# Kernel tuning notes

Hardware: AMD Instinct MI355X
Metric: run time of the kernel (lower is better)

## Reference

```python
import jax, jax.numpy as jnp
import numpy as np

HC = 4
C = 256
TMAX = 20
RMS_EPS = 1e-6
PRE_EPS = 0.0
SINKHORN_EPS = 1e-6
POST_MULT = 2.0


def setup_inputs() -> dict:
    key = jax.random.key(0)
    k1, k2, k3 = jax.random.split(key, 3)
    B, S = 8, 4096
    m = HC * HC + 2 * HC
    x = jax.random.normal(k1, (B, S, HC, C), dtype=jnp.float32)
    phi = jax.random.normal(k2, (HC * C, m), dtype=jnp.float32) * 0.02
    b = jnp.zeros((m,), dtype=jnp.float32)
    W = jax.random.normal(k3, (C, C), dtype=jnp.float32) * (1.0 / np.sqrt(C))
    return {
        "x": x, "phi": phi, "b": b,
        "alpha_pre": jnp.float32(1.0), "alpha_post": jnp.float32(1.0), "alpha_res": jnp.float32(1.0),
        "W": W,
    }


def _mhc_coeffs(x, phi, b, alpha_pre, alpha_post, alpha_res):
    # x: [..., HC, C] -> flatten streams, project, RMS-normalize logits.
    lead = x.shape[:-2]
    v = x.reshape(lead + (HC * C,))
    logits = jnp.einsum('...k,km->...m', v, phi)            # [..., m]
    rms = jnp.sqrt(jnp.mean(logits * logits, axis=-1, keepdims=True) + RMS_EPS)
    y = logits / rms + b                                     # [..., m]
    pre = y[..., :HC]
    post = y[..., HC:2 * HC]
    res = y[..., 2 * HC:].reshape(lead + (HC, HC))
    h_pre = jax.nn.sigmoid(alpha_pre * pre) + PRE_EPS        # [..., HC]
    h_post = POST_MULT * jax.nn.sigmoid(alpha_post * post)   # [..., HC]
    # Sinkhorn-Knopp: make exp(alpha_res * res) approximately doubly stochastic.
    P = jnp.exp(alpha_res * res)                             # [..., HC, HC]

    def step(P, _):
        P = P / (jnp.sum(P, axis=-1, keepdims=True) + SINKHORN_EPS)  # row norm
        P = P / (jnp.sum(P, axis=-2, keepdims=True) + SINKHORN_EPS)  # col norm
        return P, None

    P, _ = jax.lax.scan(step, P, None, length=TMAX)
    return h_pre, h_post, P


def reference(x, phi, b, alpha_pre, alpha_post, alpha_res, W):
    h_pre, h_post, h_res = _mhc_coeffs(x, phi, b, alpha_pre, alpha_post, alpha_res)
    # Pre-aggregate streams: x_in = sum_i h_pre[i] * x[i]
    x_in = jnp.einsum('...i,...ic->...c', h_pre, x)          # [..., C]
    # Wrapped layer: nn.Linear(C, C, bias=False) -> x_in @ W.T
    f_out = x_in @ W.T                                       # [..., C]
    # Post + residual: x_out[o] = sum_i h_res[o,i]*x[i] + h_post[o]*f_out
    x_out = jnp.einsum('...oi,...ic->...oc', h_res, x) + h_post[..., :, None] * f_out[..., None, :]
    return x_out
```

## Files before the change

kernel.cpp:

```cpp
#include <hip/hip_runtime.h>

typedef __attribute__((ext_vector_type(4))) float floatx4;
typedef __attribute__((ext_vector_type(8))) short short8;

__device__ __forceinline__ unsigned short f2bf(float f) {
    union { float f; unsigned int i; } v; v.f = f;
    unsigned int x = v.i;
    unsigned int r = (x + 0x7FFFu + ((x >> 16) & 1u)) >> 16;
    return (unsigned short)r;
}
__device__ __forceinline__ float bf2f(unsigned short u) {
    union { unsigned int i; float f; } v; v.i = ((unsigned int)u) << 16;
    return v.f;
}

__global__ void mhc_prep(const float* __restrict__ phi, const float* __restrict__ W,
                         unsigned short* __restrict__ phiF, unsigned short* __restrict__ WF) {
    int e = blockIdx.x * 256 + threadIdx.x;
    if (e < 32768) {
        int j = e & 7, lane = (e >> 3) & 63, nt = (e >> 9) & 1, ks = e >> 10;
        int n = nt * 16 + (lane & 15);
        int k = ks * 32 + ((lane >> 4) & 3) * 8 + j;
        float v = (n < 24) ? phi[k * 24 + n] : 0.0f;
        phiF[e] = f2bf(v);
    } else {
        int e2 = e - 32768;
        int j = e2 & 7, lane = (e2 >> 3) & 63, ks = (e2 >> 9) & 7, nt = e2 >> 12;
        int n = nt * 16 + (lane & 15);
        int k = ks * 32 + ((lane >> 4) & 3) * 8 + j;
        WF[e2] = f2bf(W[n * 256 + k]);
    }
}

#define XS_STRIDE 1032
#define XIN_STRIDE 264
#define CO_STRIDE 28

__global__ __launch_bounds__(256) void mhc_main(
    const float* __restrict__ x, const float* __restrict__ bias,
    const float* __restrict__ s_ap, const float* __restrict__ s_apo,
    const float* __restrict__ s_ar,
    const unsigned short* __restrict__ phiF, const unsigned short* __restrict__ WF,
    float* __restrict__ out)
{
    __shared__ unsigned short xs[16 * XS_STRIDE];
    __shared__ unsigned short xin[16 * XIN_STRIDE];
    __shared__ float lg[16 * CO_STRIDE];
    __shared__ float coef[16 * CO_STRIDE];

    const int t = threadIdx.x;
    const int lane = t & 63;
    const int w = t >> 6;
    const int quad = lane >> 4;
    const int col = lane & 15;
    const long base = (long)blockIdx.x * (16 * 1024);

    {
        const float4* xg = (const float4*)(x + base);
        #pragma unroll
        for (int ii = 0; ii < 16; ++ii) {
            int lin = ii * 256 + t;
            float4 v = xg[lin];
            int tok = lin >> 8;
            int k = (lin & 255) * 4;
            uint2 pk;
            pk.x = (unsigned int)f2bf(v.x) | ((unsigned int)f2bf(v.y) << 16);
            pk.y = (unsigned int)f2bf(v.z) | ((unsigned int)f2bf(v.w) << 16);
            *reinterpret_cast<uint2*>(&xs[tok * XS_STRIDE + k]) = pk;
        }
    }
    __syncthreads();

    if (w < 2) {
        floatx4 acc = {0.0f, 0.0f, 0.0f, 0.0f};
        for (int ks = 0; ks < 32; ++ks) {
            short8 a = *reinterpret_cast<const short8*>(&xs[col * XS_STRIDE + ks * 32 + quad * 8]);
            short8 b = *reinterpret_cast<const short8*>(&phiF[(ks * 2 + w) * 512 + lane * 8]);
            acc = __builtin_amdgcn_mfma_f32_16x16x32_bf16(a, b, acc, 0, 0, 0);
        }
        int n = w * 16 + col;
        if (n < 24) {
            #pragma unroll
            for (int r = 0; r < 4; ++r)
                lg[(quad * 4 + r) * CO_STRIDE + n] = acc[r];
        }
    }
    __syncthreads();

    {
        int g = t >> 4, p = t & 15;
        float a = lg[g * CO_STRIDE + p];
        float b2 = (p < 8) ? lg[g * CO_STRIDE + 16 + p] : 0.0f;
        float s = a * a + b2 * b2;
        s += __shfl_xor(s, 1); s += __shfl_xor(s, 2);
        s += __shfl_xor(s, 4); s += __shfl_xor(s, 8);
        float rinv = 1.0f / sqrtf(s * (1.0f / 24.0f) + 1e-6f);
        float yP = lg[g * CO_STRIDE + 8 + p] * rinv + bias[8 + p];
        float P = expf(s_ar[0] * yP);
        for (int it = 0; it < 20; ++it) {
            float r = P + __shfl_xor(P, 1); r += __shfl_xor(r, 2);
            P *= __builtin_amdgcn_rcpf(r + 1e-6f);
            float c = P + __shfl_xor(P, 4); c += __shfl_xor(c, 8);
            P *= __builtin_amdgcn_rcpf(c + 1e-6f);
        }
        coef[g * CO_STRIDE + 8 + p] = P;
        if (p < 8) {
            float yh = a * rinv + bias[p];
            float h = (p < 4) ? 1.0f / (1.0f + expf(-s_ap[0] * yh))
                              : 2.0f / (1.0f + expf(-s_apo[0] * yh));
            coef[g * CO_STRIDE + p] = h;
        }
    }
    __syncthreads();

    {
        int c = t;
        #pragma unroll 4
        for (int tok = 0; tok < 16; ++tok) {
            float4 h4 = *reinterpret_cast<const float4*>(&coef[tok * CO_STRIDE]);
            const unsigned short* xr = &xs[tok * XS_STRIDE + c];
            float s = h4.x * bf2f(xr[0]) + h4.y * bf2f(xr[256])
                    + h4.z * bf2f(xr[512]) + h4.w * bf2f(xr[768]);
            xin[tok * XIN_STRIDE + c] = f2bf(s);
        }
    }
    __syncthreads();

    short8 afr[8];
    #pragma unroll
    for (int ks = 0; ks < 8; ++ks)
        afr[ks] = *reinterpret_cast<const short8*>(&xin[col * XIN_STRIDE + ks * 32 + quad * 8]);
    floatx4 accs[4];
    #pragma unroll
    for (int nt = 0; nt < 4; ++nt) {
        floatx4 acc = {0.0f, 0.0f, 0.0f, 0.0f};
        int ntile = w * 4 + nt;
        #pragma unroll
        for (int ks = 0; ks < 8; ++ks) {
            short8 b = *reinterpret_cast<const short8*>(&WF[(ntile * 8 + ks) * 512 + lane * 8]);
            acc = __builtin_amdgcn_mfma_f32_16x16x32_bf16(afr[ks], b, acc, 0, 0, 0);
        }
        accs[nt] = acc;
    }

    #pragma unroll
    for (int r = 0; r < 4; ++r) {
        int tok = quad * 4 + r;
        const float* cb = &coef[tok * CO_STRIDE];
        float4 hpo = *reinterpret_cast<const float4*>(cb + 4);
        float4 P0  = *reinterpret_cast<const float4*>(cb + 8);
        float4 P1  = *reinterpret_cast<const float4*>(cb + 12);
        float4 P2  = *reinterpret_cast<const float4*>(cb + 16);
        float4 P3  = *reinterpret_cast<const float4*>(cb + 20);
        long ob = base + (long)tok * 1024;
        #pragma unroll
        for (int nt = 0; nt < 4; ++nt) {
            int c = (w * 4 + nt) * 16 + col;
            float f = accs[nt][r];
            const unsigned short* xr = &xs[tok * XS_STRIDE + c];
            float x0 = bf2f(xr[0]),   x1 = bf2f(xr[256]);
            float x2 = bf2f(xr[512]), x3 = bf2f(xr[768]);
            out[ob + c]       = P0.x * x0 + P0.y * x1 + P0.z * x2 + P0.w * x3 + hpo.x * f;
            out[ob + 256 + c] = P1.x * x0 + P1.y * x1 + P1.z * x2 + P1.w * x3 + hpo.y * f;
            out[ob + 512 + c] = P2.x * x0 + P2.y * x1 + P2.z * x2 + P2.w * x3 + hpo.z * f;
            out[ob + 768 + c] = P3.x * x0 + P3.y * x1 + P3.z * x2 + P3.w * x3 + hpo.w * f;
        }
    }
}

extern "C" void kernel_launch(void* const* d_in, const int* in_sizes, int n_in,
                              void* d_out, int out_size, void* d_ws, size_t ws_size,
                              hipStream_t stream) {
    const float* x    = (const float*)d_in[0];
    const float* phi  = (const float*)d_in[1];
    const float* bias = (const float*)d_in[2];
    const float* ap   = (const float*)d_in[3];
    const float* apo  = (const float*)d_in[4];
    const float* ar   = (const float*)d_in[5];
    const float* W    = (const float*)d_in[6];
    float* out = (float*)d_out;

    unsigned short* phiF = (unsigned short*)d_ws;
    unsigned short* WF   = (unsigned short*)d_ws + 32768;

    mhc_prep<<<384, 256, 0, stream>>>(phi, W, phiF, WF);
    mhc_main<<<2048, 256, 0, stream>>>(x, bias, ap, apo, ar, phiF, WF, out);
}
```

Before: 262.9 us.

## Keep x in fp32 registers, split logits GEMM across warps, vectorize output stores

Each warp now loads four tokens of x into fp32 registers and reuses them for both pre-aggregation and the residual mix. This removes the bf16 LDS round trip and improves accuracy. The logits GEMM is split over all four warps along K, with partial sums added afterwards. Sinkhorn now runs on 4 lanes per token, each holding one row in registers, so row sums need no shuffles. The GEMM output is staged through LDS that aliases the x buffer, so the epilogue can write contiguous float4 nontemporal stores. The cost is more register pressure (launch_bounds 256,3) and extra barriers.

```diff
diff --git a/kernel.cpp b/kernel.cpp
--- a/kernel.cpp
+++ b/kernel.cpp
@@ -1,17 +1,22 @@
 #include <hip/hip_runtime.h>
+#include <hip/hip_bf16.h>
 
 typedef __attribute__((ext_vector_type(4))) float floatx4;
 typedef __attribute__((ext_vector_type(8))) short short8;
 
 __device__ __forceinline__ unsigned short f2bf(float f) {
     union { float f; unsigned int i; } v; v.f = f;
-    unsigned int x = v.i;
-    unsigned int r = (x + 0x7FFFu + ((x >> 16) & 1u)) >> 16;
+    unsigned int r = (v.i + 0x7FFFu + ((v.i >> 16) & 1u)) >> 16;
     return (unsigned short)r;
 }
-__device__ __forceinline__ float bf2f(unsigned short u) {
-    union { unsigned int i; float f; } v; v.i = ((unsigned int)u) << 16;
-    return v.f;
+
+__device__ __forceinline__ uint2 pack_bf16x4(float4 v) {
+    __hip_bfloat162 lo = __float22bfloat162_rn(make_float2(v.x, v.y));
+    __hip_bfloat162 hi = __float22bfloat162_rn(make_float2(v.z, v.w));
+    uint2 r;
+    __builtin_memcpy(&r.x, &lo, 4);
+    __builtin_memcpy(&r.y, &hi, 4);
+    return r;
 }
 
 __global__ void mhc_prep(const float* __restrict__ phi, const float* __restrict__ W,
@@ -21,8 +26,7 @@
         int j = e & 7, lane = (e >> 3) & 63, nt = (e >> 9) & 1, ks = e >> 10;
         int n = nt * 16 + (lane & 15);
         int k = ks * 32 + ((lane >> 4) & 3) * 8 + j;
-        float v = (n < 24) ? phi[k * 24 + n] : 0.0f;
-        phiF[e] = f2bf(v);
+        phiF[e] = f2bf((n < 24) ? phi[k * 24 + n] : 0.0f);
     } else {
         int e2 = e - 32768;
         int j = e2 & 7, lane = (e2 >> 3) & 63, ks = (e2 >> 9) & 7, nt = e2 >> 12;
@@ -34,137 +38,180 @@
 
 #define XS_STRIDE 1032
 #define XIN_STRIDE 264
-#define CO_STRIDE 28
-
-__global__ __launch_bounds__(256) void mhc_main(
+#define FO_STRIDE 260
+#define CO_STRIDE 24
+
+__global__ __launch_bounds__(256, 3) void mhc_main(
     const float* __restrict__ x, const float* __restrict__ bias,
     const float* __restrict__ s_ap, const float* __restrict__ s_apo,
     const float* __restrict__ s_ar,
     const unsigned short* __restrict__ phiF, const unsigned short* __restrict__ WF,
     float* __restrict__ out)
 {
-    __shared__ unsigned short xs[16 * XS_STRIDE];
-    __shared__ unsigned short xin[16 * XIN_STRIDE];
-    __shared__ float lg[16 * CO_STRIDE];
-    __shared__ float coef[16 * CO_STRIDE];
+    __shared__ __align__(16) unsigned char smem[16 * XS_STRIDE * 2];
+    __shared__ __align__(16) float lgp[2][16 * CO_STRIDE];
+    __shared__ __align__(16) float lgy[16 * CO_STRIDE];
+    __shared__ __align__(16) float coef[16 * CO_STRIDE];
+
+    unsigned short* xs  = (unsigned short*)smem;
+    unsigned short* xin = (unsigned short*)smem;
+    float*          fo  = (float*)(smem + 16 * XIN_STRIDE * 2);
 
     const int t = threadIdx.x;
     const int lane = t & 63;
     const int w = t >> 6;
     const int quad = lane >> 4;
     const int col = lane & 15;
-    const long base = (long)blockIdx.x * (16 * 1024);
+    const int tok0 = w * 4;
+    const int c4 = lane * 4;
+    const long base = (long)blockIdx.x * 16384;
+
+    float4 xr[4][4];
+    #pragma unroll
+    for (int tk = 0; tk < 4; ++tk)
+        #pragma unroll
+        for (int i = 0; i < 4; ++i)
+            xr[tk][i] = *reinterpret_cast<const float4*>(
+                x + base + (long)(tok0 + tk) * 1024 + i * 256 + c4);
+    #pragma unroll
+    for (int tk = 0; tk < 4; ++tk)
+        #pragma unroll
+        for (int i = 0; i < 4; ++i)
+            *reinterpret_cast<uint2*>(&xs[(tok0 + tk) * XS_STRIDE + i * 256 + c4]) =
+                pack_bf16x4(xr[tk][i]);
+    __syncthreads();
 
     {
-        const float4* xg = (const float4*)(x + base);
-        #pragma unroll
-        for (int ii = 0; ii < 16; ++ii) {
-            int lin = ii * 256 + t;
-            float4 v = xg[lin];
-            int tok = lin >> 8;
-            int k = (lin & 255) * 4;
-            uint2 pk;
-            pk.x = (unsigned int)f2bf(v.x) | ((unsigned int)f2bf(v.y) << 16);
-            pk.y = (unsigned int)f2bf(v.z) | ((unsigned int)f2bf(v.w) << 16);
-            *reinterpret_cast<uint2*>(&xs[tok * XS_STRIDE + k]) = pk;
-        }
-    }
-    __syncthreads();
-
-    if (w < 2) {
+        int nt = w & 1, half = w >> 1;
         floatx4 acc = {0.0f, 0.0f, 0.0f, 0.0f};
-        for (int ks = 0; ks < 32; ++ks) {
+        #pragma unroll
+        for (int kk = 0; kk < 16; ++kk) {
+            int ks = half * 16 + kk;
             short8 a = *reinterpret_cast<const short8*>(&xs[col * XS_STRIDE + ks * 32 + quad * 8]);
-            short8 b = *reinterpret_cast<const short8*>(&phiF[(ks * 2 + w) * 512 + lane * 8]);
+            short8 b = *reinterpret_cast<const short8*>(&phiF[(ks * 2 + nt) * 512 + lane * 8]);
             acc = __builtin_amdgcn_mfma_f32_16x16x32_bf16(a, b, acc, 0, 0, 0);
         }
-        int n = w * 16 + col;
+        int n = nt * 16 + col;
         if (n < 24) {
             #pragma unroll
             for (int r = 0; r < 4; ++r)
-                lg[(quad * 4 + r) * CO_STRIDE + n] = acc[r];
+                lgp[half][(quad * 4 + r) * CO_STRIDE + n] = acc[r];
         }
     }
     __syncthreads();
 
     {
-        int g = t >> 4, p = t & 15;
-        float a = lg[g * CO_STRIDE + p];
-        float b2 = (p < 8) ? lg[g * CO_STRIDE + 16 + p] : 0.0f;
-        float s = a * a + b2 * b2;
+        int tok = t >> 4, p = t & 15;
+        float ya = lgp[0][tok * CO_STRIDE + p] + lgp[1][tok * CO_STRIDE + p];
+        float yb = (p < 8) ? (lgp[0][tok * CO_STRIDE + 16 + p] + lgp[1][tok * CO_STRIDE + 16 + p])
+                           : 0.0f;
+        float s = ya * ya + yb * yb;
         s += __shfl_xor(s, 1); s += __shfl_xor(s, 2);
         s += __shfl_xor(s, 4); s += __shfl_xor(s, 8);
-        float rinv = 1.0f / sqrtf(s * (1.0f / 24.0f) + 1e-6f);
-        float yP = lg[g * CO_STRIDE + 8 + p] * rinv + bias[8 + p];
-        float P = expf(s_ar[0] * yP);
+        float rinv = __builtin_amdgcn_rsqf(s * (1.0f / 24.0f) + 1e-6f);
+        float yp = ya * rinv + bias[p];
+        lgy[tok * CO_STRIDE + p] = yp;
+        if (p < 8) {
+            lgy[tok * CO_STRIDE + 16 + p] = yb * rinv + bias[16 + p];
+            float a = (p < 4) ? s_ap[0] : s_apo[0];
+            float h = __builtin_amdgcn_rcpf(1.0f + __builtin_amdgcn_exp2f(-a * yp * 1.44269504f));
+            if (p >= 4) h *= 2.0f;
+            coef[tok * CO_STRIDE + p] = h;
+        }
+    }
+    __syncthreads();
+
+    if ((t & 15) < 4) {
+        int tok = t >> 4, o = t & 3;
+        float arl = s_ar[0] * 1.44269504f;
+        float4 yv = *reinterpret_cast<const float4*>(&lgy[tok * CO_STRIDE + 8 + o * 4]);
+        float4 P;
+        P.x = __builtin_amdgcn_exp2f(arl * yv.x);
+        P.y = __builtin_amdgcn_exp2f(arl * yv.y);
+        P.z = __builtin_amdgcn_exp2f(arl * yv.z);
+        P.w = __builtin_amdgcn_exp2f(arl * yv.w);
+        #pragma unroll 1
         for (int it = 0; it < 20; ++it) {
-            float r = P + __shfl_xor(P, 1); r += __shfl_xor(r, 2);
-            P *= __builtin_amdgcn_rcpf(r + 1e-6f);
-            float c = P + __shfl_xor(P, 4); c += __shfl_xor(c, 8);
-            P *= __builtin_amdgcn_rcpf(c + 1e-6f);
-        }
-        coef[g * CO_STRIDE + 8 + p] = P;
-        if (p < 8) {
-            float yh = a * rinv + bias[p];
-            float h = (p < 4) ? 1.0f / (1.0f + expf(-s_ap[0] * yh))
-                              : 2.0f / (1.0f + expf(-s_apo[0] * yh));
-            coef[g * CO_STRIDE + p] = h;
-        }
+            float ri = __builtin_amdgcn_rcpf(P.x + P.y + P.z + P.w + 1e-6f);
+            P.x *= ri; P.y *= ri; P.z *= ri; P.w *= ri;
+            float cx = P.x + __shfl_xor(P.x, 1); cx += __shfl_xor(cx, 2);
+            float cy = P.y + __shfl_xor(P.y, 1); cy += __shfl_xor(cy, 2);
+            float cz = P.z + __shfl_xor(P.z, 1); cz += __shfl_xor(cz, 2);
+            float cw = P.w + __shfl_xor(P.w, 1); cw += __shfl_xor(cw, 2);
+            P.x *= __builtin_amdgcn_rcpf(cx + 1e-6f);
+            P.y *= __builtin_amdgcn_rcpf(cy + 1e-6f);
+            P.z *= __builtin_amdgcn_rcpf(cz + 1e-6f);
+            P.w *= __builtin_amdgcn_rcpf(cw + 1e-6f);
+        }
+        *reinterpret_cast<float4*>(&coef[tok * CO_STRIDE + 8 + o * 4]) = P;
+    }
+
+    #pragma unroll
+    for (int tk = 0; tk < 4; ++tk) {
+        const float* cb = &coef[(tok0 + tk) * CO_STRIDE];
+        float hx = cb[0], hy = cb[1], hz = cb[2], hw = cb[3];
+        float4 xi;
+        xi.x = hx * xr[tk][0].x + hy * xr[tk][1].x + hz * xr[tk][2].x + hw * xr[tk][3].x;
+        xi.y = hx * xr[tk][0].y + hy * xr[tk][1].y + hz * xr[tk][2].y + hw * xr[tk][3].y;
+        xi.z = hx * xr[tk][0].z + hy * xr[tk][1].z + hz * xr[tk][2].z + hw * xr[tk][3].z;
+        xi.w = hx * xr[tk][0].w + hy * xr[tk][1].w + hz * xr[tk][2].w + hw * xr[tk][3].w;
+        *reinterpret_cast<uint2*>(&xin[(tok0 + tk) * XIN_STRIDE + c4]) = pack_bf16x4(xi);
     }
     __syncthreads();
 
     {
-        int c = t;
-        #pragma unroll 4
-        for (int tok = 0; tok < 16; ++tok) {
-            float4 h4 = *reinterpret_cast<const float4*>(&coef[tok * CO_STRIDE]);
-            const unsigned short* xr = &xs[tok * XS_STRIDE + c];
-            float s = h4.x * bf2f(xr[0]) + h4.y * bf2f(xr[256])
-                    + h4.z * bf2f(xr[512]) + h4.w * bf2f(xr[768]);
-            xin[tok * XIN_STRIDE + c] = f2bf(s);
-        }
-    }
-    __syncthreads();
-
-    short8 afr[8];
-    #pragma unroll
-    for (int ks = 0; ks < 8; ++ks)
-        afr[ks] = *reinterpret_cast<const short8*>(&xin[col * XIN_STRIDE + ks * 32 + quad * 8]);
-    floatx4 accs[4];
-    #pragma unroll
-    for (int nt = 0; nt < 4; ++nt) {
-        floatx4 acc = {0.0f, 0.0f, 0.0f, 0.0f};
-        int ntile = w * 4 + nt;
-        #pragma unroll
-        for (int ks = 0; ks < 8; ++ks) {
-            short8 b = *reinterpret_cast<const short8*>(&WF[(ntile * 8 + ks) * 512 + lane * 8]);
-            acc = __builtin_amdgcn_mfma_f32_16x16x32_bf16(afr[ks], b, acc, 0, 0, 0);
-        }
-        accs[nt] = acc;
-    }
-
-    #pragma unroll
-    for (int r = 0; r < 4; ++r) {
-        int tok = quad * 4 + r;
+        short8 afr[8];
+        #pragma unroll
+        for (int ks = 0; ks < 8; ++ks)
+            afr[ks] = *reinterpret_cast<const short8*>(&xin[col * XIN_STRIDE + ks * 32 + quad * 8]);
+        #pragma unroll
+        for (int nt = 0; nt < 4; ++nt) {
+            floatx4 acc = {0.0f, 0.0f, 0.0f, 0.0f};
+            int ntile = w * 4 + nt;
+            #pragma unroll
+            for (int ks = 0; ks < 8; ++ks) {
+                short8 b = *reinterpret_cast<const short8*>(&WF[(ntile * 8 + ks) * 512 + lane * 8]);
+                acc = __builtin_amdgcn_mfma_f32_16x16x32_bf16(afr[ks], b, acc, 0, 0, 0);
+            }
+            #pragma unroll
+            for (int r = 0; r < 4; ++r)
+                fo[(quad * 4 + r) * FO_STRIDE + ntile * 16 + col] = acc[r];
+        }
+    }
+    __syncthreads();
+
+    #pragma unroll
+    for (int tk = 0; tk < 4; ++tk) {
+        int tok = tok0 + tk;
         const float* cb = &coef[tok * CO_STRIDE];
+        float4 f   = *reinterpret_cast<const float4*>(&fo[tok * FO_STRIDE + c4]);
         float4 hpo = *reinterpret_cast<const float4*>(cb + 4);
         float4 P0  = *reinterpret_cast<const float4*>(cb + 8);
         float4 P1  = *reinterpret_cast<const float4*>(cb + 12);
         float4 P2  = *reinterpret_cast<const float4*>(cb + 16);
         float4 P3  = *reinterpret_cast<const float4*>(cb + 20);
-        long ob = base + (long)tok * 1024;
-        #pragma unroll
-        for (int nt = 0; nt < 4; ++nt) {
-            int c = (w * 4 + nt) * 16 + col;
-            float f = accs[nt][r];
-            const unsigned short* xr = &xs[tok * XS_STRIDE + c];
-            float x0 = bf2f(xr[0]),   x1 = bf2f(xr[256]);
-            float x2 = bf2f(xr[512]), x3 = bf2f(xr[768]);
-            out[ob + c]       = P0.x * x0 + P0.y * x1 + P0.z * x2 + P0.w * x3 + hpo.x * f;
-            out[ob + 256 + c] = P1.x * x0 + P1.y * x1 + P1.z * x2 + P1.w * x3 + hpo.y * f;
-            out[ob + 512 + c] = P2.x * x0 + P2.y * x1 + P2.z * x2 + P2.w * x3 + hpo.z * f;
-            out[ob + 768 + c] = P3.x * x0 + P3.y * x1 + P3.z * x2 + P3.w * x3 + hpo.w * f;
-        }
+        float* ob = out + base + (long)tok * 1024 + c4;
+        floatx4 o0, o1, o2, o3;
+        o0.x = P0.x*xr[tk][0].x + P0.y*xr[tk][1].x + P0.z*xr[tk][2].x + P0.w*xr[tk][3].x + hpo.x*f.x;
+        o0.y = P0.x*xr[tk][0].y + P0.y*xr[tk][1].y + P0.z*xr[tk][2].y + P0.w*xr[tk][3].y + hpo.x*f.y;
+        o0.z = P0.x*xr[tk][0].z + P0.y*xr[tk][1].z + P0.z*xr[tk][2].z + P0.w*xr[tk][3].z + hpo.x*f.z;
+        o0.w = P0.x*xr[tk][0].w + P0.y*xr[tk][1].w + P0.z*xr[tk][2].w + P0.w*xr[tk][3].w + hpo.x*f.w;
+        o1.x = P1.x*xr[tk][0].x + P1.y*xr[tk][1].x + P1.z*xr[tk][2].x + P1.w*xr[tk][3].x + hpo.y*f.x;
+        o1.y = P1.x*xr[tk][0].y + P1.y*xr[tk][1].y + P1.z*xr[tk][2].y + P1.w*xr[tk][3].y + hpo.y*f.y;
+        o1.z = P1.x*xr[tk][0].z + P1.y*xr[tk][1].z + P1.z*xr[tk][2].z + P1.w*xr[tk][3].z + hpo.y*f.z;
+        o1.w = P1.x*xr[tk][0].w + P1.y*xr[tk][1].w + P1.z*xr[tk][2].w + P1.w*xr[tk][3].w + hpo.y*f.w;
+        o2.x = P2.x*xr[tk][0].x + P2.y*xr[tk][1].x + P2.z*xr[tk][2].x + P2.w*xr[tk][3].x + hpo.z*f.x;
+        o2.y = P2.x*xr[tk][0].y + P2.y*xr[tk][1].y + P2.z*xr[tk][2].y + P2.w*xr[tk][3].y + hpo.z*f.y;
+        o2.z = P2.x*xr[tk][0].z + P2.y*xr[tk][1].z + P2.z*xr[tk][2].z + P2.w*xr[tk][3].z + hpo.z*f.z;
+        o2.w = P2.x*xr[tk][0].w + P2.y*xr[tk][1].w + P2.z*xr[tk][2].w + P2.w*xr[tk][3].w + hpo.z*f.w;
+        o3.x = P3.x*xr[tk][0].x + P3.y*xr[tk][1].x + P3.z*xr[tk][2].x + P3.w*xr[tk][3].x + hpo.w*f.x;
+        o3.y = P3.x*xr[tk][0].y + P3.y*xr[tk][1].y + P3.z*xr[tk][2].y + P3.w*xr[tk][3].y + hpo.w*f.y;
+        o3.z = P3.x*xr[tk][0].z + P3.y*xr[tk][1].z + P3.z*xr[tk][2].z + P3.w*xr[tk][3].z + hpo.w*f.z;
+        o3.w = P3.x*xr[tk][0].w + P3.y*xr[tk][1].w + P3.z*xr[tk][2].w + P3.w*xr[tk][3].w + hpo.w*f.w;
+        __builtin_nontemporal_store(o0, reinterpret_cast<floatx4*>(ob));
+        __builtin_nontemporal_store(o1, reinterpret_cast<floatx4*>(ob + 256));
+        __builtin_nontemporal_store(o2, reinterpret_cast<floatx4*>(ob + 512));
+        __builtin_nontemporal_store(o3, reinterpret_cast<floatx4*>(ob + 768));
     }
 }
 
```

Measured after the change: 264.4 us. About the same (+0.5%).
